# Optimization experiments

Measured on AMD Instinct MI355X. Metric: run time of the kernel, lower is better.

Reference implementation:

```python
import jax, jax.numpy as jnp
import numpy as np

NHEAD = 16
HEAD_DIM = 64
ROPE_BASE = 10000.0


def _rotate_half(x):
    # interleaved convention: pairs (x0,x1)->(-x1,x0)
    x1 = x[..., ::2]
    x2 = x[..., 1::2]
    return jnp.stack([-x2, x1], axis=-1).reshape(x.shape)


def _rope_cache(seq_len, head_dim, base):
    half = head_dim // 2
    inv_freq = 1.0 / base ** (jnp.arange(half, dtype=jnp.float32) / float(half))
    t = jnp.arange(seq_len, dtype=jnp.float32)
    freqs = jnp.einsum('i,j->ij', t, inv_freq)          # [T, half]
    emb = jnp.concatenate([freqs, freqs], axis=-1)      # [T, D] (half-half cat, matches torch source)
    return jnp.cos(emb), jnp.sin(emb)


def setup_inputs() -> dict:
    key = jax.random.key(0)
    k1, k2, k3 = jax.random.split(key, 3)
    b, t, c = 2, 2048, 1024
    x = jax.random.normal(k1, (b, t, c), dtype=jnp.float32)
    # torch nn.Linear weights: [out_features, in_features], scaled like kaiming-uniform-ish
    W_qkv = jax.random.normal(k2, (3 * c, c), dtype=jnp.float32) / np.sqrt(c)
    W_out = jax.random.normal(k3, (c, c), dtype=jnp.float32) / np.sqrt(c)
    return {"x": x, "W_qkv": W_qkv, "W_out": W_out}


def reference(x, W_qkv, W_out):
    b, t, c = x.shape
    nh, hd = NHEAD, HEAD_DIM
    qkv = x @ W_qkv.T                                   # [b, t, 3c]
    q, k, v = jnp.split(qkv, 3, axis=-1)

    def to_heads(a):
        return a.reshape(b, t, nh, hd).transpose(0, 2, 1, 3)  # [b, nh, t, hd]

    q, k, v = to_heads(q), to_heads(k), to_heads(v)
    cos, sin = _rope_cache(t, hd, ROPE_BASE)            # [t, hd]
    cos = cos.astype(q.dtype)[None, None]
    sin = sin.astype(q.dtype)[None, None]
    q = q * cos + _rotate_half(q) * sin
    k = k * cos + _rotate_half(k) * sin

    scale = 1.0 / np.sqrt(hd).astype(np.float32)
    scores = jnp.einsum('bhqd,bhkd->bhqk', q, k) * scale
    attn = jax.nn.softmax(scores, axis=-1)
    y = jnp.einsum('bhqk,bhkd->bhqd', attn, v)          # [b, nh, t, hd]
    y = y.transpose(0, 2, 1, 3).reshape(b, t, c)
    return y @ W_out.T
```

## Files before the change

kernel.cpp:

```cpp
#include <hip/hip_runtime.h>
#include <hip/hip_bf16.h>
#include <math.h>

typedef __hip_bfloat16 bf16;
typedef _Float16 f16;
typedef __attribute__((ext_vector_type(8))) short bf16x8;
typedef __attribute__((ext_vector_type(8))) _Float16 f16x8;
typedef __attribute__((ext_vector_type(4))) float f32x4;
typedef __attribute__((ext_vector_type(4))) unsigned u32x4;

#define MFMA_BF(a,b,c) __builtin_amdgcn_mfma_f32_16x16x32_bf16((a),(b),(c),0,0,0)
#define MFMA_F16(a,b,c) __builtin_amdgcn_mfma_f32_16x16x32_f16((a),(b),(c),0,0,0)

__device__ __forceinline__ void load_lds16(const void* g, void* l) {
  __builtin_amdgcn_global_load_lds(
      (__attribute__((address_space(1))) void*)(g),
      (__attribute__((address_space(3))) void*)(l), 16, 0, 0);
}

__device__ __forceinline__ unsigned pk_bf16(float a, float b) {
  unsigned ua = __builtin_bit_cast(unsigned, a);
  unsigned ub = __builtin_bit_cast(unsigned, b);
  ua += 0x7fffu + ((ua >> 16) & 1u);
  ub += 0x7fffu + ((ub >> 16) & 1u);
  return (ua >> 16) | (ub & 0xffff0000u);
}

__global__ void cvt_all(const float* __restrict__ x, const float* __restrict__ wq,
                        const float* __restrict__ wo, unsigned* __restrict__ xb,
                        unsigned* __restrict__ wqb, unsigned* __restrict__ wob) {
  int i = blockIdx.x * blockDim.x + threadIdx.x;
  const float* src;
  unsigned* dst;
  int off;
  if (i < 1048576) { src = x; dst = xb; off = i; }
  else if (i < 1048576 + 786432) { src = wq; dst = wqb; off = i - 1048576; }
  else { src = wo; dst = wob; off = i - (1048576 + 786432); }
  float4 v = reinterpret_cast<const float4*>(src)[off];
  uint2 u;
  u.x = pk_bf16(v.x, v.y);
  u.y = pk_bf16(v.z, v.w);
  reinterpret_cast<uint2*>(dst)[off] = u;
}

__global__ __launch_bounds__(256, 2)
void gemm_qkv(const bf16* __restrict__ A, const bf16* __restrict__ B,
              bf16* __restrict__ outq, bf16* __restrict__ outk,
              f16* __restrict__ outv) {
  __shared__ __align__(16) bf16 As[128 * 32];
  __shared__ __align__(16) bf16 Bs[128 * 32];
  const int K = 1024;
  const int tid = threadIdx.x;
  const int w = tid >> 6;
  const int lane = tid & 63;
  const int quad = lane >> 4;
  const int col = lane & 15;
  const int waveM = w >> 1;
  const int waveN = w & 1;
  const int bm = blockIdx.y * 128;
  const int bn = blockIdx.x * 128;

  f32x4 acc[4][4] = {};
  const int srow = lane >> 2;
  const int skoff = (lane & 3) * 8;

  for (int k0 = 0; k0 < K; k0 += 32) {
    __syncthreads();
#pragma unroll
    for (int p = 0; p < 2; ++p) {
      int r = p * 64 + w * 16 + srow;
      load_lds16(A + (size_t)(bm + r) * K + k0 + skoff, (char*)As + p * 4096 + w * 1024);
      load_lds16(B + (size_t)(bn + r) * K + k0 + skoff, (char*)Bs + p * 4096 + w * 1024);
    }
    __syncthreads();
    bf16x8 af[4], bfr[4];
#pragma unroll
    for (int i = 0; i < 4; ++i)
      af[i] = *reinterpret_cast<const bf16x8*>(As + (waveM * 64 + i * 16 + col) * 32 + quad * 8);
#pragma unroll
    for (int j = 0; j < 4; ++j)
      bfr[j] = *reinterpret_cast<const bf16x8*>(Bs + (waveN * 64 + j * 16 + col) * 32 + quad * 8);
#pragma unroll
    for (int i = 0; i < 4; ++i)
#pragma unroll
      for (int j = 0; j < 4; ++j)
        acc[i][j] = MFMA_BF(af[i], bfr[j], acc[i][j]);
  }

  if (bn < 2048) {
    const float NEGK = -0.4152410118f;
    const float C1 = 0.1803368799f;
    const float sgn = (col & 1) ? 1.0f : -1.0f;
#pragma unroll
    for (int j = 0; j < 4; ++j) {
      const int n0 = bn + waveN * 64 + j * 16;
      const int sel = n0 >> 10;
      const int hh = (n0 & 1023) >> 6;
      const int dd = (n0 & 63) + col;
      bf16* outp = sel ? outk : outq;
      const float post = sel ? 1.0f : C1;
      const float invf = __builtin_amdgcn_exp2f((float)((n0 & 31) + col) * NEGK);
#pragma unroll
      for (int i = 0; i < 4; ++i) {
#pragma unroll
        for (int r = 0; r < 4; ++r) {
          int m = bm + waveM * 64 + i * 16 + quad * 4 + r;
          int b = m >> 11, t = m & 2047;
          float v = acc[i][j][r];
          float partner = __shfl_xor(v, 1);
          float ang = (float)t * invf;
          float res = (v * __cosf(ang) + sgn * partner * __sinf(ang)) * post;
          outp[((size_t)(b * 16 + hh) * 2048 + t) * 64 + dd] = __float2bfloat16(res);
        }
      }
    }
  } else {
    const int b = bm >> 11;
    const int tt0 = (bm & 2047) + waveM * 64;
#pragma unroll
    for (int j = 0; j < 4; ++j) {
      const int n0 = bn + waveN * 64 + j * 16;
      const int hh = (n0 & 1023) >> 6;
      const int dd = (n0 & 63) + col;
      f16* dst = outv + (size_t)(b * 16 + hh) * 131072 + (size_t)dd * 2048;
#pragma unroll
      for (int i = 0; i < 4; ++i) {
        uint2 pk;
        pk.x = __builtin_bit_cast(unsigned, __builtin_amdgcn_cvt_pkrtz(acc[i][j][0], acc[i][j][1]));
        pk.y = __builtin_bit_cast(unsigned, __builtin_amdgcn_cvt_pkrtz(acc[i][j][2], acc[i][j][3]));
        *reinterpret_cast<uint2*>(dst + tt0 + i * 16 + quad * 4) = pk;
      }
    }
  }
}

__global__ __launch_bounds__(256, 2)
void gemm_out(const bf16* __restrict__ A, const bf16* __restrict__ B,
              float* __restrict__ outf) {
  __shared__ __align__(16) bf16 As[64 * 32];
  __shared__ __align__(16) bf16 Bs[128 * 32];
  const int K = 1024;
  const int tid = threadIdx.x;
  const int w = tid >> 6;
  const int lane = tid & 63;
  const int quad = lane >> 4;
  const int col = lane & 15;
  const int bm = blockIdx.y * 64;
  const int bn = blockIdx.x * 128;

  f32x4 acc[4][2] = {};
  const int srow = lane >> 2;
  const int skoff = (lane & 3) * 8;

  for (int k0 = 0; k0 < K; k0 += 32) {
    __syncthreads();
    load_lds16(A + (size_t)(bm + w * 16 + srow) * K + k0 + skoff, (char*)As + w * 1024);
#pragma unroll
    for (int p = 0; p < 2; ++p)
      load_lds16(B + (size_t)(bn + p * 64 + w * 16 + srow) * K + k0 + skoff,
                 (char*)Bs + p * 4096 + w * 1024);
    __syncthreads();
    bf16x8 af[4], bfr[2];
#pragma unroll
    for (int i = 0; i < 4; ++i)
      af[i] = *reinterpret_cast<const bf16x8*>(As + (i * 16 + col) * 32 + quad * 8);
#pragma unroll
    for (int j = 0; j < 2; ++j)
      bfr[j] = *reinterpret_cast<const bf16x8*>(Bs + (w * 32 + j * 16 + col) * 32 + quad * 8);
#pragma unroll
    for (int i = 0; i < 4; ++i)
#pragma unroll
      for (int j = 0; j < 2; ++j)
        acc[i][j] = MFMA_BF(af[i], bfr[j], acc[i][j]);
  }

#pragma unroll
  for (int i = 0; i < 4; ++i)
#pragma unroll
    for (int j = 0; j < 2; ++j) {
      const int n0 = bn + w * 32 + j * 16;
#pragma unroll
      for (int r = 0; r < 4; ++r) {
        int m = bm + i * 16 + quad * 4 + r;
        outf[(size_t)m * 1024 + n0 + col] = acc[i][j][r];
      }
    }
}

__global__ __launch_bounds__(256, 4)
void attn_kernel(const bf16* __restrict__ qh, const bf16* __restrict__ kh,
                 const f16* __restrict__ vt, bf16* __restrict__ O1,
                 bf16* __restrict__ O2, float* __restrict__ lw) {
  __shared__ __align__(16) bf16 Ks[2][64 * 64];
  __shared__ __align__(16) f16 Vs[2][64 * 64];

  const int bh = blockIdx.z;
  const int split = blockIdx.y;
  const int kc0 = split << 10;
  const int w = threadIdx.x >> 6;
  const int lane = threadIdx.x & 63;
  const int quad = lane >> 4;
  const int col = lane & 15;

  const int qrow0 = blockIdx.x * 128 + w * 32 + col;
  bf16x8 qf[2][2];
#pragma unroll
  for (int f = 0; f < 2; ++f)
#pragma unroll
    for (int c = 0; c < 2; ++c)
      qf[f][c] = *reinterpret_cast<const bf16x8*>(
          qh + ((size_t)bh * 2048 + qrow0 + f * 16) * 64 + c * 32 + quad * 8);

  const int s8 = lane >> 3;
  const int blk = (lane & 7) ^ s8;
  const bf16* kg = kh + (size_t)bh * 2048 * 64;
  const f16* vg = vt + (size_t)bh * 64 * 2048;
  char* klds0 = (char*)&Ks[0][0] + w * 2048;
  char* vlds0 = (char*)&Vs[0][0] + w * 2048;
  const int ks0 = 32 * (w >> 1) + 8 * ((4 * w + (s8 >> 2)) & 3) + 4 * (w & 1) + (s8 & 3);
  const int ks1 = 32 * (w >> 1) + 8 * ((4 * w + 2 + (s8 >> 2)) & 3) + 4 * (w & 1) + (s8 & 3);
  const int vrow0 = w * 16 + s8;

  const int csw = col & 7;
  const int sw0 = (quad ^ csw) * 8;
  const int sw1 = ((quad + 4) ^ csw) * 8;
  const int rdbase = col * 64;

  f32x4 O[2][4] = {};
  float l[2] = {};

  load_lds16(kg + (size_t)(kc0 + ks0) * 64 + blk * 8, klds0);
  load_lds16(kg + (size_t)(kc0 + ks1) * 64 + blk * 8, klds0 + 1024);
  load_lds16(vg + (size_t)vrow0 * 2048 + kc0 + blk * 8, vlds0);
  load_lds16(vg + (size_t)(vrow0 + 8) * 2048 + kc0 + blk * 8, vlds0 + 1024);

  int buf = 0;
  const int kend = kc0 + 1024;
  for (int kc = kc0; kc < kend; kc += 64) {
    __asm__ volatile("s_waitcnt vmcnt(0)" ::: "memory");
    __asm__ volatile("s_barrier" ::: "memory");
    if (kc + 64 < kend) {
      const int nb = buf ^ 1;
      const int kn = kc + 64;
      load_lds16(kg + (size_t)(kn + ks0) * 64 + blk * 8, klds0 + nb * 8192);
      load_lds16(kg + (size_t)(kn + ks1) * 64 + blk * 8, klds0 + nb * 8192 + 1024);
      load_lds16(vg + (size_t)vrow0 * 2048 + kn + blk * 8, vlds0 + nb * 8192);
      load_lds16(vg + (size_t)(vrow0 + 8) * 2048 + kn + blk * 8, vlds0 + nb * 8192 + 1024);
    }

    const bf16* kt = &Ks[buf][0];
    const f16* vtile = &Vs[buf][0];

    f32x4 s[2][4];
#pragma unroll
    for (int t = 0; t < 4; ++t) {
      bf16x8 kf0 = *reinterpret_cast<const bf16x8*>(kt + t * 1024 + rdbase + sw0);
      bf16x8 kf1 = *reinterpret_cast<const bf16x8*>(kt + t * 1024 + rdbase + sw1);
#pragma unroll
      for (int f = 0; f < 2; ++f) {
        f32x4 a = {};
        a = MFMA_BF(kf0, qf[f][0], a);
        a = MFMA_BF(kf1, qf[f][1], a);
        s[f][t] = a;
      }
    }

    f16x8 pf[2][2];
#pragma unroll
    for (int f = 0; f < 2; ++f) {
      unsigned pk[8];
      float lf = 0.0f;
#pragma unroll
      for (int t = 0; t < 4; ++t) {
        float p0 = __builtin_amdgcn_exp2f(s[f][t][0]);
        float p1 = __builtin_amdgcn_exp2f(s[f][t][1]);
        float p2 = __builtin_amdgcn_exp2f(s[f][t][2]);
        float p3 = __builtin_amdgcn_exp2f(s[f][t][3]);
        lf += (p0 + p1) + (p2 + p3);
        pk[t * 2]     = __builtin_bit_cast(unsigned, __builtin_amdgcn_cvt_pkrtz(p0, p1));
        pk[t * 2 + 1] = __builtin_bit_cast(unsigned, __builtin_amdgcn_cvt_pkrtz(p2, p3));
      }
      l[f] += lf;
      pf[f][0] = __builtin_bit_cast(f16x8, (u32x4){pk[0], pk[1], pk[2], pk[3]});
      pf[f][1] = __builtin_bit_cast(f16x8, (u32x4){pk[4], pk[5], pk[6], pk[7]});
    }

#pragma unroll
    for (int j = 0; j < 4; ++j) {
      f16x8 vf0 = *reinterpret_cast<const f16x8*>(vtile + j * 1024 + rdbase + sw0);
      f16x8 vf1 = *reinterpret_cast<const f16x8*>(vtile + j * 1024 + rdbase + sw1);
#pragma unroll
      for (int f = 0; f < 2; ++f) {
        O[f][j] = MFMA_F16(vf0, pf[f][0], O[f][j]);
        O[f][j] = MFMA_F16(vf1, pf[f][1], O[f][j]);
      }
    }
    buf ^= 1;
  }

  bf16* o_out = split ? O2 : O1;
  float* lrow = lw + split * 65536 + bh * 2048;
  const int b = bh >> 4, h = bh & 15;
#pragma unroll
  for (int f = 0; f < 2; ++f) {
    float lv = l[f];
    lv += __shfl_xor(lv, 16, 64);
    lv += __shfl_xor(lv, 32, 64);
    int tq = blockIdx.x * 128 + w * 32 + f * 16 + col;
    if (lane < 16) lrow[tq] = lv;
    size_t base = ((size_t)b * 2048 + tq) * 1024 + h * 64;
#pragma unroll
    for (int j = 0; j < 4; ++j) {
      uint2 pk2;
      pk2.x = pk_bf16(O[f][j][0], O[f][j][1]);
      pk2.y = pk_bf16(O[f][j][2], O[f][j][3]);
      *reinterpret_cast<uint2*>((unsigned short*)o_out + base + j * 16 + quad * 4) = pk2;
    }
  }
}

__global__ void merge_y(const bf16* __restrict__ O1, const bf16* __restrict__ O2,
                        const float* __restrict__ lw, bf16* __restrict__ y) {
  int i = blockIdx.x * blockDim.x + threadIdx.x;
  int c8 = i & 127;
  int t = (i >> 7) & 2047;
  int b = i >> 18;
  int bh = b * 16 + (c8 >> 3);
  float inv = 1.0f / (lw[bh * 2048 + t] + lw[65536 + bh * 2048 + t]);
  size_t off = (size_t)i * 8;
  ushort4 a1 = *reinterpret_cast<const ushort4*>((const unsigned short*)O1 + off);
  ushort4 a2 = *reinterpret_cast<const ushort4*>((const unsigned short*)O2 + off);
  ushort4 b1 = *reinterpret_cast<const ushort4*>((const unsigned short*)O1 + off + 4);
  ushort4 b2 = *reinterpret_cast<const ushort4*>((const unsigned short*)O2 + off + 4);
  const unsigned short* u1 = &a1.x;
  const unsigned short* u2 = &a2.x;
  const unsigned short* v1 = &b1.x;
  const unsigned short* v2 = &b2.x;
  float o[8];
#pragma unroll
  for (int e = 0; e < 4; ++e) {
    float s1 = __builtin_bit_cast(float, (unsigned)u1[e] << 16) +
               __builtin_bit_cast(float, (unsigned)u2[e] << 16);
    float s2 = __builtin_bit_cast(float, (unsigned)v1[e] << 16) +
               __builtin_bit_cast(float, (unsigned)v2[e] << 16);
    o[e] = s1 * inv;
    o[e + 4] = s2 * inv;
  }
  uint4 res;
  res.x = pk_bf16(o[0], o[1]);
  res.y = pk_bf16(o[2], o[3]);
  res.z = pk_bf16(o[4], o[5]);
  res.w = pk_bf16(o[6], o[7]);
  *reinterpret_cast<uint4*>((unsigned short*)y + off) = res;
}

extern "C" void kernel_launch(void* const* d_in, const int* in_sizes, int n_in,
                              void* d_out, int out_size, void* d_ws, size_t ws_size,
                              hipStream_t stream) {
  const float* x    = (const float*)d_in[0];
  const float* wqkv = (const float*)d_in[1];
  const float* wout = (const float*)d_in[2];
  float* out = (float*)d_out;
  char* ws = (char*)d_ws;

  bf16* xb    = (bf16*)(ws);
  bf16* wqkvb = (bf16*)(ws + (size_t)(8 << 20));
  bf16* woutb = (bf16*)(ws + (size_t)(14 << 20));
  bf16* qh    = (bf16*)(ws + (size_t)(16 << 20));
  bf16* kh    = (bf16*)(ws + (size_t)(24 << 20));
  f16*  vt    = (f16*) (ws + (size_t)(32 << 20));
  bf16* O1    = (bf16*)(ws + (size_t)(40 << 20));
  bf16* O2    = (bf16*)(ws);
  float* lw   = (float*)(ws + (size_t)(8 << 20));
  bf16* y     = (bf16*)(ws + (size_t)(16 << 20));

  cvt_all<<<8192, 256, 0, stream>>>(x, wqkv, wout,
                                    (unsigned*)xb, (unsigned*)wqkvb, (unsigned*)woutb);
  gemm_qkv<<<dim3(24, 32), 256, 0, stream>>>(xb, wqkvb, qh, kh, vt);
  attn_kernel<<<dim3(16, 2, 32), 256, 0, stream>>>(qh, kh, vt, O1, O2, lw);
  merge_y<<<2048, 256, 0, stream>>>(O1, O2, lw, y);
  gemm_out<<<dim3(8, 64), 256, 0, stream>>>(y, woutb, out);
}
```

Measured before the change: 198.4 us.

## Double-buffer LDS tiles and XOR-swizzle layout in both GEMM kernels

Both projection GEMMs now keep two LDS buffers, issuing the global-to-LDS loads for the next K tile before computing on the current one, so each iteration needs one barrier instead of two. Each thread's source column chunk is XOR-permuted by row while the LDS destination stays fixed, and the fragment reads apply the same permutation, to cut LDS bank conflicts. The cost is double the LDS per block, which may lower occupancy. There is also a possible hazard: the waitcnt and barrier sit at the top of each iteration and no second barrier follows the compute, so a fast wave could begin overwriting a buffer that slower waves are still reading.

After: 196.9 us. Within noise of the previous version (-0.8%).

```diff
diff --git a/kernel.cpp b/kernel.cpp
--- a/kernel.cpp
+++ b/kernel.cpp
@@ -47,8 +47,8 @@
 void gemm_qkv(const bf16* __restrict__ A, const bf16* __restrict__ B,
               bf16* __restrict__ outq, bf16* __restrict__ outk,
               f16* __restrict__ outv) {
-  __shared__ __align__(16) bf16 As[128 * 32];
-  __shared__ __align__(16) bf16 Bs[128 * 32];
+  __shared__ __align__(16) bf16 As[2][128 * 32];
+  __shared__ __align__(16) bf16 Bs[2][128 * 32];
   const int K = 1024;
   const int tid = threadIdx.x;
   const int w = tid >> 6;
@@ -62,29 +62,46 @@
 
   f32x4 acc[4][4] = {};
   const int srow = lane >> 2;
-  const int skoff = (lane & 3) * 8;
-
+  const int skoff = (((lane & 3) ^ ((srow >> 1) & 3))) * 8;
+  const int swq = (quad ^ ((col >> 1) & 3)) * 8;
+
+#pragma unroll
+  for (int p = 0; p < 2; ++p) {
+    int r = p * 64 + w * 16 + srow;
+    load_lds16(A + (size_t)(bm + r) * K + skoff, (char*)As + p * 4096 + w * 1024);
+    load_lds16(B + (size_t)(bn + r) * K + skoff, (char*)Bs + p * 4096 + w * 1024);
+  }
+
+  int buf = 0;
   for (int k0 = 0; k0 < K; k0 += 32) {
-    __syncthreads();
-#pragma unroll
-    for (int p = 0; p < 2; ++p) {
-      int r = p * 64 + w * 16 + srow;
-      load_lds16(A + (size_t)(bm + r) * K + k0 + skoff, (char*)As + p * 4096 + w * 1024);
-      load_lds16(B + (size_t)(bn + r) * K + k0 + skoff, (char*)Bs + p * 4096 + w * 1024);
-    }
-    __syncthreads();
+    __asm__ volatile("s_waitcnt vmcnt(0)" ::: "memory");
+    __asm__ volatile("s_barrier" ::: "memory");
+    if (k0 + 32 < K) {
+      const int nb = buf ^ 1;
+#pragma unroll
+      for (int p = 0; p < 2; ++p) {
+        int r = p * 64 + w * 16 + srow;
+        load_lds16(A + (size_t)(bm + r) * K + k0 + 32 + skoff,
+                   (char*)As + nb * 8192 + p * 4096 + w * 1024);
+        load_lds16(B + (size_t)(bn + r) * K + k0 + 32 + skoff,
+                   (char*)Bs + nb * 8192 + p * 4096 + w * 1024);
+      }
+    }
+    const bf16* at = &As[buf][0];
+    const bf16* bt = &Bs[buf][0];
     bf16x8 af[4], bfr[4];
 #pragma unroll
     for (int i = 0; i < 4; ++i)
-      af[i] = *reinterpret_cast<const bf16x8*>(As + (waveM * 64 + i * 16 + col) * 32 + quad * 8);
+      af[i] = *reinterpret_cast<const bf16x8*>(at + (waveM * 64 + i * 16 + col) * 32 + swq);
 #pragma unroll
     for (int j = 0; j < 4; ++j)
-      bfr[j] = *reinterpret_cast<const bf16x8*>(Bs + (waveN * 64 + j * 16 + col) * 32 + quad * 8);
+      bfr[j] = *reinterpret_cast<const bf16x8*>(bt + (waveN * 64 + j * 16 + col) * 32 + swq);
 #pragma unroll
     for (int i = 0; i < 4; ++i)
 #pragma unroll
       for (int j = 0; j < 4; ++j)
         acc[i][j] = MFMA_BF(af[i], bfr[j], acc[i][j]);
+    buf ^= 1;
   }
 
   if (bn < 2048) {
@@ -137,8 +154,8 @@
 __global__ __launch_bounds__(256, 2)
 void gemm_out(const bf16* __restrict__ A, const bf16* __restrict__ B,
               float* __restrict__ outf) {
-  __shared__ __align__(16) bf16 As[64 * 32];
-  __shared__ __align__(16) bf16 Bs[128 * 32];
+  __shared__ __align__(16) bf16 As[2][64 * 32];
+  __shared__ __align__(16) bf16 Bs[2][128 * 32];
   const int K = 1024;
   const int tid = threadIdx.x;
   const int w = tid >> 6;
@@ -150,28 +167,43 @@
 
   f32x4 acc[4][2] = {};
   const int srow = lane >> 2;
-  const int skoff = (lane & 3) * 8;
-
+  const int skoff = (((lane & 3) ^ ((srow >> 1) & 3))) * 8;
+  const int swq = (quad ^ ((col >> 1) & 3)) * 8;
+
+  load_lds16(A + (size_t)(bm + w * 16 + srow) * K + skoff, (char*)As + w * 1024);
+#pragma unroll
+  for (int p = 0; p < 2; ++p)
+    load_lds16(B + (size_t)(bn + p * 64 + w * 16 + srow) * K + skoff,
+               (char*)Bs + p * 4096 + w * 1024);
+
+  int buf = 0;
   for (int k0 = 0; k0 < K; k0 += 32) {
-    __syncthreads();
-    load_lds16(A + (size_t)(bm + w * 16 + srow) * K + k0 + skoff, (char*)As + w * 1024);
-#pragma unroll
-    for (int p = 0; p < 2; ++p)
-      load_lds16(B + (size_t)(bn + p * 64 + w * 16 + srow) * K + k0 + skoff,
-                 (char*)Bs + p * 4096 + w * 1024);
-    __syncthreads();
+    __asm__ volatile("s_waitcnt vmcnt(0)" ::: "memory");
+    __asm__ volatile("s_barrier" ::: "memory");
+    if (k0 + 32 < K) {
+      const int nb = buf ^ 1;
+      load_lds16(A + (size_t)(bm + w * 16 + srow) * K + k0 + 32 + skoff,
+                 (char*)As + nb * 4096 + w * 1024);
+#pragma unroll
+      for (int p = 0; p < 2; ++p)
+        load_lds16(B + (size_t)(bn + p * 64 + w * 16 + srow) * K + k0 + 32 + skoff,
+                   (char*)Bs + nb * 8192 + p * 4096 + w * 1024);
+    }
+    const bf16* at = &As[buf][0];
+    const bf16* bt = &Bs[buf][0];
     bf16x8 af[4], bfr[2];
 #pragma unroll
     for (int i = 0; i < 4; ++i)
-      af[i] = *reinterpret_cast<const bf16x8*>(As + (i * 16 + col) * 32 + quad * 8);
+      af[i] = *reinterpret_cast<const bf16x8*>(at + (i * 16 + col) * 32 + swq);
 #pragma unroll
     for (int j = 0; j < 2; ++j)
-      bfr[j] = *reinterpret_cast<const bf16x8*>(Bs + (w * 32 + j * 16 + col) * 32 + quad * 8);
+      bfr[j] = *reinterpret_cast<const bf16x8*>(bt + (w * 32 + j * 16 + col) * 32 + swq);
 #pragma unroll
     for (int i = 0; i < 4; ++i)
 #pragma unroll
       for (int j = 0; j < 2; ++j)
         acc[i][j] = MFMA_BF(af[i], bfr[j], acc[i][j]);
+    buf ^= 1;
   }
 
 #pragma unroll
```
